# Kernel tuning notes

Hardware: AMD Instinct MI355X
Metric: run time of the kernel (lower is better)

Reference implementation:

```python
import jax, jax.numpy as jnp
import numpy as np
import math

# Model dims (match init_kwargs)
H = 4096      # hidden_size
NH = 32       # num attention heads
NKV = 8       # num kv heads
D = 128       # head_dim
S = 2048      # num tokens
WINDOW = 1024 # sliding window (layer_idx=0 -> active)
SCALE = D ** -0.5
# YaRN rope params from GptOssConfig.rope_parameters
BASE = 500000.0
FACTOR = 4.0
ORIG_MAX = 32768
BETA_FAST = 32
BETA_SLOW = 1


def _yarn_cos_sin(positions):
    """YaRN-scaled rotary cos/sin, NEOX style. Returns ([S, D/2], [S, D/2])."""
    d2 = D // 2
    pos_freqs = BASE ** (np.arange(d2, dtype=np.float64) * 2.0 / D)
    inv_extra = 1.0 / pos_freqs
    inv_inter = 1.0 / (FACTOR * pos_freqs)

    def corr_dim(n):
        return (D * math.log(ORIG_MAX / (n * 2 * math.pi))) / (2 * math.log(BASE))

    low = max(math.floor(corr_dim(BETA_FAST)), 0)
    high = min(math.ceil(corr_dim(BETA_SLOW)), d2 - 1)
    ramp = np.clip((np.arange(d2, dtype=np.float64) - low) / max(high - low, 0.001), 0.0, 1.0)
    mask = 1.0 - ramp  # 1 -> extrapolation (high freq), 0 -> interpolation (low freq)
    inv_freq = inv_inter * (1.0 - mask) + inv_extra * mask
    mscale = 0.1 * math.log(FACTOR) + 1.0
    freqs = positions.astype(jnp.float32)[:, None] * jnp.asarray(inv_freq, dtype=jnp.float32)[None, :]
    return jnp.cos(freqs) * mscale, jnp.sin(freqs) * mscale


def _rope(x, cos, sin):
    # x: [S, h, D]; rotate-halves (NEOX)
    x1, x2 = jnp.split(x, 2, axis=-1)
    c, s = cos[:, None, :], sin[:, None, :]
    return jnp.concatenate([x1 * c - x2 * s, x2 * c + x1 * s], axis=-1)


def reference(hidden_states, positions, qkv_w, qkv_b, o_w, o_b, sinks):
    qs, kvs = NH * D, NKV * D
    qkv = hidden_states @ qkv_w.T + qkv_b                  # [S, qs + 2*kvs]
    q = qkv[:, :qs].reshape(S, NH, D)
    k = qkv[:, qs:qs + kvs].reshape(S, NKV, D)
    v = qkv[:, qs + kvs:].reshape(S, NKV, D)

    cos, sin = _yarn_cos_sin(positions)
    q = _rope(q, cos, sin)
    k = _rope(k, cos, sin)

    # GQA: expand kv heads to match q heads
    g = NH // NKV
    k = jnp.repeat(k, g, axis=1)                            # [S, NH, D]
    v = jnp.repeat(v, g, axis=1)

    scores = jnp.einsum('qhd,khd->hqk', q, k) * SCALE       # [NH, S, S]
    i = jnp.arange(S)[:, None]
    j = jnp.arange(S)[None, :]
    allowed = (j <= i) & ((i - j) < WINDOW)                 # causal + sliding window
    scores = jnp.where(allowed[None, :, :], scores, -jnp.inf)

    # sink-aware softmax: learned per-head sink logit joins the normalization
    m = jnp.maximum(jnp.max(scores, axis=-1), sinks[:, None])   # [NH, S]
    e = jnp.exp(scores - m[..., None])                          # masked -> exp(-inf)=0
    denom = e.sum(-1) + jnp.exp(sinks[:, None] - m)             # [NH, S]
    probs = e / denom[..., None]

    attn = jnp.einsum('hqk,khd->qhd', probs, v).reshape(S, NH * D)
    return attn @ o_w.T + o_b


def setup_inputs() -> dict:
    key = jax.random.key(0)
    k1, k2, k3, k4, k5 = jax.random.split(key, 5)
    w_scale = 0.02
    return {
        'hidden_states': jax.random.normal(k1, (S, H), dtype=jnp.float32),
        'positions': jnp.arange(S, dtype=jnp.int64) if jax.config.jax_enable_x64 else jnp.arange(S, dtype=jnp.int32),
        'qkv_w': jax.random.normal(k2, (NH * D + 2 * NKV * D, H), dtype=jnp.float32) * w_scale,
        'qkv_b': jax.random.normal(k3, (NH * D + 2 * NKV * D,), dtype=jnp.float32) * w_scale,
        'o_w': jax.random.normal(k4, (H, H), dtype=jnp.float32) * w_scale,
        'o_b': jax.random.normal(k5, (H,), dtype=jnp.float32) * w_scale,
        'sinks': jnp.zeros((NH,), dtype=jnp.float32),
    }
```

## Files before the change

### kernel.cpp

```cpp
#include <hip/hip_runtime.h>

#define S_LEN   2048
#define HID     4096
#define NH      32
#define NKV     8
#define HD      128
#define QKV_N   (NH*HD + 2*NKV*HD)
#define WINDOW  1024

typedef unsigned short u16;
typedef short s8v  __attribute__((ext_vector_type(8)));
typedef short s4v  __attribute__((ext_vector_type(4)));
typedef float f4v  __attribute__((ext_vector_type(4)));

#define MFMA16x32(a, b, c) __builtin_amdgcn_mfma_f32_16x16x32_bf16(a, b, c, 0, 0, 0)

typedef __attribute__((address_space(1))) const unsigned int g_u32;
typedef __attribute__((address_space(3))) unsigned int l_u32;

__device__ __forceinline__ float bf2f(u16 h) {
  union { unsigned int u; float f; } x;
  x.u = ((unsigned int)h) << 16;
  return x.f;
}
__device__ __forceinline__ u16 f2bf(float f) {
  union { float f; unsigned int u; } x;
  x.f = f;
  unsigned int u = x.u;
  return (u16)((u + 0x7FFFu + ((u >> 16) & 1u)) >> 16);
}

__global__ __launch_bounds__(256) void cvt_bf16(const float* __restrict__ in,
                                               u16* __restrict__ out) {
  int i = (blockIdx.x * 256 + threadIdx.x) * 4;
  float4 v = *(const float4*)&in[i];
  u16 h[4] = { f2bf(v.x), f2bf(v.y), f2bf(v.z), f2bf(v.w) };
  *(s4v*)&out[i] = *(const s4v*)h;
}

__global__ __launch_bounds__(256) void cvt_fused(
    const float* __restrict__ hidden, const float* __restrict__ qkv_w,
    u16* __restrict__ hb, u16* __restrict__ wW) {
  int b = blockIdx.x;
  const float* in;
  u16* out;
  int i;
  if (b < 24576) { in = qkv_w;  out = wW; i = (b * 256 + threadIdx.x) * 4; }
  else           { in = hidden; out = hb; i = ((b - 24576) * 256 + threadIdx.x) * 4; }
  float4 v = *(const float4*)&in[i];
  u16 h[4] = { f2bf(v.x), f2bf(v.y), f2bf(v.z), f2bf(v.w) };
  *(s4v*)&out[i] = *(const s4v*)h;
}

template<int OUT_BF16>
__global__ __launch_bounds__(512, 4) void gemm_bt(
    const u16* __restrict__ A, const u16* __restrict__ B,
    const float* __restrict__ bias, void* __restrict__ Cp,
    int M, int N, int K)
{
  __shared__ __align__(16) char lds[3 * 24576];
  const int tid  = threadIdx.x;
  const int lane = tid & 63;
  const int w    = tid >> 6;
  const int wm   = w >> 2, wn = w & 3;
  const int ln   = lane & 15, quad = lane >> 4;
  const long mBase = (long)blockIdx.y * 128;
  const long nBase = (long)blockIdx.x * 256;
  const u16* Ab = A + mBase * (long)K;
  const u16* Bb = B + nBase * (long)K;
  const long rs = (long)K * 2;

  f4v acc[4][4];
#pragma unroll
  for (int i = 0; i < 4; ++i)
#pragma unroll
    for (int j = 0; j < 4; ++j)
#pragma unroll
      for (int r = 0; r < 4; ++r) acc[i][j][r] = 0.0f;

  const int nt = K >> 5;

  auto stage = [&](int tile) {
    char* base = lds + (tile % 3) * 24576;
    const int ktb = tile * 64;
#pragma unroll
    for (int k = 0; k < 3; ++k) {
      const u16* gsrc = (k == 0) ? Ab : Bb;
      char* ldst      = (k == 0) ? base : (base + 8192);
      const int kk    = (k == 0) ? 0 : (k - 1);
      int o  = kk * 8192 + w * 1024 + lane * 16;
      int o2 = o ^ ((o >> 3) & 0x30);
      const char* gp = (const char*)gsrc + (long)(o2 >> 6) * rs + ktb + (o2 & 63);
      __builtin_amdgcn_global_load_lds((g_u32*)(const void*)gp,
                                       (l_u32*)(void*)(ldst + kk * 8192 + w * 1024),
                                       16, 0, 0);
    }
  };

  stage(0);
  stage(1);
  asm volatile("s_waitcnt vmcnt(3)" ::: "memory");
  __builtin_amdgcn_s_barrier();
  __builtin_amdgcn_sched_barrier(0);

  int bsel = 0;
  for (int t = 0; t < nt; ++t) {
    char* base = lds + bsel * 24576;
    if (t + 2 < nt) stage(t + 2);

    __builtin_amdgcn_s_setprio(1);
    s8v af[4], bf[4];
#pragma unroll
    for (int f = 0; f < 4; ++f) {
      int r = wm * 64 + f * 16 + ln;
      int o = r * 64 + quad * 16;
      o ^= (o >> 3) & 0x30;
      af[f] = *(const s8v*)(base + o);
    }
#pragma unroll
    for (int j = 0; j < 4; ++j) {
      int r = wn * 64 + j * 16 + ln;
      int o = r * 64 + quad * 16;
      o ^= (o >> 3) & 0x30;
      bf[j] = *(const s8v*)(base + 8192 + o);
    }
#pragma unroll
    for (int i = 0; i < 4; ++i)
#pragma unroll
      for (int j = 0; j < 4; ++j)
        acc[i][j] = MFMA16x32(af[i], bf[j], acc[i][j]);
    __builtin_amdgcn_s_setprio(0);

    if (t < nt - 2) {
      asm volatile("s_waitcnt vmcnt(3)" ::: "memory");
      __builtin_amdgcn_s_barrier();
      __builtin_amdgcn_sched_barrier(0);
    } else if (t == nt - 2) {
      asm volatile("s_waitcnt vmcnt(0)" ::: "memory");
      __builtin_amdgcn_s_barrier();
      __builtin_amdgcn_sched_barrier(0);
    }
    bsel = (bsel == 2) ? 0 : bsel + 1;
  }

#pragma unroll
  for (int i = 0; i < 4; ++i) {
    long rowb = mBase + wm * 64 + i * 16 + quad * 4;
#pragma unroll
    for (int j = 0; j < 4; ++j) {
      long col = nBase + wn * 64 + j * 16 + ln;
      float bv = bias[col];
#pragma unroll
      for (int r = 0; r < 4; ++r) {
        float v = acc[i][j][r] + bv;
        if (OUT_BF16) ((u16*)Cp)[(rowb + r) * (long)N + col] = f2bf(v);
        else          ((float*)Cp)[(rowb + r) * (long)N + col] = v;
      }
    }
  }
}

__global__ __launch_bounds__(256) void rope_split(
    const u16* __restrict__ qkv, const int* __restrict__ positions,
    u16* __restrict__ qo, u16* __restrict__ ko, u16* __restrict__ vo)
{
  const int s = blockIdx.x;
  const int t = threadIdx.x;
  __shared__ float csh[64], snh[64];

  if (t < 64) {
    const double LN_BASE = log(500000.0);
    const double TWO_PI  = 6.283185307179586476925287;
    double cf  = 128.0 * log(32768.0 / (32.0 * TWO_PI)) / (2.0 * LN_BASE);
    double cs_ = 128.0 * log(32768.0 / TWO_PI) / (2.0 * LN_BASE);
    double lowd  = floor(cf);  if (lowd < 0.0)  lowd = 0.0;
    double highd = ceil(cs_);  if (highd > 63.0) highd = 63.0;
    double denom = highd - lowd; if (denom < 0.001) denom = 0.001;
    double d = (double)t;
    double inv_extra = exp(-LN_BASE * d / 64.0);
    double inv_inter = inv_extra * 0.25;
    double ramp = (d - lowd) / denom;
    ramp = ramp < 0.0 ? 0.0 : (ramp > 1.0 ? 1.0 : ramp);
    double maskv = 1.0 - ramp;
    double invf = inv_inter * (1.0 - maskv) + inv_extra * maskv;
    float freq = (float)positions[s] * (float)invf;
    const float msc = 1.1386294361119891f;
    csh[t] = cosf(freq) * msc;
    snh[t] = sinf(freq) * msc;
  }
  __syncthreads();

  const u16* row = qkv + (size_t)s * QKV_N;
  const float SC = 0.08838834764831845f;

#pragma unroll
  for (int i = 0; i < 8; ++i) {
    int p = i * 256 + t;
    int hh = p >> 6, d = p & 63;
    float x1 = bf2f(row[hh * 128 + d]), x2 = bf2f(row[hh * 128 + d + 64]);
    float c = csh[d], sn = snh[d];
    qo[(size_t)s * 4096 + hh * 128 + d]      = f2bf((x1 * c - x2 * sn) * SC);
    qo[(size_t)s * 4096 + hh * 128 + d + 64] = f2bf((x2 * c + x1 * sn) * SC);
  }
#pragma unroll
  for (int i = 0; i < 2; ++i) {
    int p = i * 256 + t;
    int hh = p >> 6, d = p & 63;
    float x1 = bf2f(row[4096 + hh * 128 + d]), x2 = bf2f(row[4096 + hh * 128 + d + 64]);
    float c = csh[d], sn = snh[d];
    ko[(size_t)s * 1024 + hh * 128 + d]      = f2bf(x1 * c - x2 * sn);
    ko[(size_t)s * 1024 + hh * 128 + d + 64] = f2bf(x2 * c + x1 * sn);
  }
#pragma unroll
  for (int i = 0; i < 4; ++i) {
    int e = i * 256 + t;
    vo[(size_t)s * 1024 + e] = row[5120 + e];
  }
}

__global__ __launch_bounds__(256) void transpose_v(const u16* __restrict__ vb,
                                                   u16* __restrict__ vt) {
  __shared__ u16 tile[64][72];
  const int s0 = blockIdx.x * 64, c0 = blockIdx.y * 64;
  const int tid = threadIdx.x;
#pragma unroll
  for (int t = 0; t < 2; ++t) {
    int row = t * 32 + (tid >> 3), col = (tid & 7) * 8;
    *(s8v*)&tile[row][col] = *(const s8v*)&vb[(size_t)(s0 + row) * 1024 + c0 + col];
  }
  __syncthreads();
#pragma unroll
  for (int t = 0; t < 2; ++t) {
    int orow = t * 32 + (tid >> 3), ocol = (tid & 7) * 8;
    u16 v[8];
#pragma unroll
    for (int e = 0; e < 8; ++e) v[e] = tile[ocol + e][orow];
    *(s8v*)&vt[(size_t)(c0 + orow) * 2048 + s0 + ocol] = *(const s8v*)v;
  }
}

__global__ __launch_bounds__(256) void attn_fwd(
    const u16* __restrict__ Q, const u16* __restrict__ Kb,
    const u16* __restrict__ Vt, const float* __restrict__ sinks,
    u16* __restrict__ O)
{
  const int h = blockIdx.y, kvh = h >> 2;
  const int q0 = blockIdx.x * 64;
  const int tid = threadIdx.x, w = tid >> 6, lane = tid & 63;
  const int ln = lane & 15, quad = lane >> 4;
  const int qw = q0 + w * 16;
  const int qi = qw + ln;

  __shared__ __align__(16) u16 sK[64 * 136];
  __shared__ __align__(16) u16 sVt[128 * 72];
  __shared__ __align__(16) u16 sP[4][16 * 72];

  s8v qf[4];
  {
    const u16* qrow = Q + (size_t)qi * 4096 + h * 128;
#pragma unroll
    for (int kb = 0; kb < 4; ++kb)
      qf[kb] = *(const s8v*)&qrow[kb * 32 + quad * 8];
  }

  float m_v = sinks[h], l_v = 1.0f;
  f4v accO[8];
#pragma unroll
  for (int j = 0; j < 8; ++j)
#pragma unroll
    for (int r = 0; r < 4; ++r) accO[j][r] = 0.0f;

  int lo = q0 - (WINDOW - 1); if (lo < 0) lo = 0; lo &= ~63;

  for (int kt = lo; kt <= q0; kt += 64) {
    __syncthreads();
#pragma unroll
    for (int t = 0; t < 4; ++t) {
      int c = t * 256 + tid;
      int row = c >> 4, col = (c & 15) * 8;
      *(s8v*)&sK[row * 136 + col] =
          *(const s8v*)&Kb[(size_t)(kt + row) * 1024 + kvh * 128 + col];
    }
#pragma unroll
    for (int t = 0; t < 4; ++t) {
      int c = t * 256 + tid;
      int row = c >> 3, col = (c & 7) * 8;
      *(s8v*)&sVt[row * 72 + col] =
          *(const s8v*)&Vt[(size_t)(kvh * 128 + row) * 2048 + kt + col];
    }
    __syncthreads();

    f4v sc[4];
    bool dead[4];
#pragma unroll
    for (int h4 = 0; h4 < 4; ++h4) {
      const int kb16 = kt + h4 * 16;
      dead[h4] = (kb16 > qw + 15) || (kb16 + 15 < qw - (WINDOW - 1));
      if (dead[h4]) {
#pragma unroll
        for (int r = 0; r < 4; ++r) sc[h4][r] = -1e30f;
        continue;
      }
      f4v s;
#pragma unroll
      for (int r = 0; r < 4; ++r) s[r] = 0.0f;
#pragma unroll
      for (int kb = 0; kb < 4; ++kb) {
        s8v kf = *(const s8v*)&sK[(h4 * 16 + ln) * 136 + kb * 32 + quad * 8];
        s = MFMA16x32(kf, qf[kb], s);
      }
      const bool full = (kb16 + 15 <= qw) && (qw + 15 - kb16 <= WINDOW - 1);
      if (!full) {
        int base = qi - kb16 - quad * 4;
#pragma unroll
        for (int r = 0; r < 4; ++r)
          s[r] = ((unsigned)(base - r) <= (WINDOW - 1)) ? s[r] : -1e30f;
      }
      sc[h4] = s;
    }

    float mn = m_v;
#pragma unroll
    for (int h4 = 0; h4 < 4; ++h4)
#pragma unroll
      for (int r = 0; r < 4; ++r) mn = fmaxf(mn, sc[h4][r]);
    mn = fmaxf(mn, __shfl_xor(mn, 16));
    mn = fmaxf(mn, __shfl_xor(mn, 32));

    float alpha = __expf(m_v - mn);
    m_v = mn;
    l_v *= alpha;
#pragma unroll
    for (int j = 0; j < 8; ++j)
#pragma unroll
      for (int r = 0; r < 4; ++r) accO[j][r] *= alpha;

    float lsum = 0.0f;
#pragma unroll
    for (int h4 = 0; h4 < 4; ++h4) {
      float p[4];
#pragma unroll
      for (int r = 0; r < 4; ++r) p[r] = __expf(sc[h4][r] - mn);
      lsum += (p[0] + p[1]) + (p[2] + p[3]);
      u16 pb[4] = { f2bf(p[0]), f2bf(p[1]), f2bf(p[2]), f2bf(p[3]) };
      *(s4v*)&sP[w][ln * 72 + h4 * 16 + quad * 4] = *(const s4v*)pb;
    }
    lsum += __shfl_xor(lsum, 16);
    lsum += __shfl_xor(lsum, 32);
    l_v += lsum;

    __syncthreads();

#pragma unroll
    for (int c2 = 0; c2 < 2; ++c2) {
      if (dead[2 * c2] && dead[2 * c2 + 1]) continue;
      s8v pf = *(const s8v*)&sP[w][ln * 72 + c2 * 32 + quad * 8];
#pragma unroll
      for (int j = 0; j < 8; ++j) {
        s8v vf = *(const s8v*)&sVt[(j * 16 + ln) * 72 + c2 * 32 + quad * 8];
        accO[j] = MFMA16x32(vf, pf, accO[j]);
      }
    }
  }

  __syncthreads();
  u16* sO = sK;
  const float rl = 1.0f / l_v;
#pragma unroll
  for (int j = 0; j < 8; ++j) {
    u16 ob[4] = { f2bf(accO[j][0] * rl), f2bf(accO[j][1] * rl),
                  f2bf(accO[j][2] * rl), f2bf(accO[j][3] * rl) };
    *(s4v*)&sO[(w * 16 + ln) * 136 + j * 16 + quad * 4] = *(const s4v*)ob;
  }
  __syncthreads();
  {
    int row = lane >> 2, cc = lane & 3;
#pragma unroll
    for (int i = 0; i < 4; ++i) {
      s8v v = *(const s8v*)&sO[(w * 16 + row) * 136 + cc * 8 + i * 32];
      *(s8v*)&O[(size_t)(q0 + w * 16 + row) * 4096 + h * 128 + cc * 8 + i * 32] = v;
    }
  }
}

extern "C" void kernel_launch(void* const* d_in, const int* in_sizes, int n_in,
                              void* d_out, int out_size, void* d_ws, size_t ws_size,
                              hipStream_t stream) {
  const float* hidden    = (const float*)d_in[0];
  const int*   positions = (const int*)d_in[1];
  const float* qkv_w     = (const float*)d_in[2];
  const float* qkv_b     = (const float*)d_in[3];
  const float* o_w       = (const float*)d_in[4];
  const float* o_b       = (const float*)d_in[5];
  const float* sinks     = (const float*)d_in[6];

  char* ws = (char*)d_ws;
  u16* wW   = (u16*)ws;
  u16* qb   = (u16*)ws;
  u16* kb   = (u16*)(ws + 16777216ull);
  u16* vb   = (u16*)(ws + 20971520ull);
  u16* vt   = (u16*)(ws + 25165824ull);
  u16* attn = (u16*)(ws + 29360128ull);
  u16* hb   = (u16*)(ws + 50331648ull);
  u16* qkvb = (u16*)(ws + 67108864ull);
  u16* oWb  = (u16*)(ws + 50331648ull);

  cvt_fused<<<32768, 256, 0, stream>>>(hidden, qkv_w, hb, wW);

  gemm_bt<1><<<dim3(QKV_N / 256, S_LEN / 128), 512, 0, stream>>>(
      hb, wW, qkv_b, (void*)qkvb, S_LEN, QKV_N, HID);

  rope_split<<<S_LEN, 256, 0, stream>>>(qkvb, positions, qb, kb, vb);

  cvt_bf16<<<16384, 256, 0, stream>>>(o_w, oWb);

  transpose_v<<<dim3(32, 16), 256, 0, stream>>>(vb, vt);

  attn_fwd<<<dim3(S_LEN / 64, NH), 256, 0, stream>>>(qb, kb, vt, sinks, attn);

  gemm_bt<0><<<dim3(HID / 256, S_LEN / 128), 512, 0, stream>>>(
      attn, oWb, o_b, d_out, S_LEN, HID, HID);
}
```

Baseline: 511.7 us.

## Prefetch next K/V tile into registers and drop redundant barriers in attention

The attention loop now loads the next K and V tile into registers while the current tile is computed, then stores them to LDS at the top of the next iteration. Block-wide syncs that only guarded per-warp LDS data are replaced with LDS waitcnts, and MFMA sections get raised wave priority. Separately, the V copy in rope_split is removed and transpose_v reads V directly from the QKV buffer, saving one pass over V. The register prefetch raises VGPR pressure and could reduce occupancy.

```diff
diff --git a/kernel.cpp b/kernel.cpp
--- a/kernel.cpp
+++ b/kernel.cpp
@@ -162,7 +162,7 @@
 
 __global__ __launch_bounds__(256) void rope_split(
     const u16* __restrict__ qkv, const int* __restrict__ positions,
-    u16* __restrict__ qo, u16* __restrict__ ko, u16* __restrict__ vo)
+    u16* __restrict__ qo, u16* __restrict__ ko)
 {
   const int s = blockIdx.x;
   const int t = threadIdx.x;
@@ -211,14 +211,9 @@
     ko[(size_t)s * 1024 + hh * 128 + d]      = f2bf(x1 * c - x2 * sn);
     ko[(size_t)s * 1024 + hh * 128 + d + 64] = f2bf(x2 * c + x1 * sn);
   }
-#pragma unroll
-  for (int i = 0; i < 4; ++i) {
-    int e = i * 256 + t;
-    vo[(size_t)s * 1024 + e] = row[5120 + e];
-  }
-}
-
-__global__ __launch_bounds__(256) void transpose_v(const u16* __restrict__ vb,
+}
+
+__global__ __launch_bounds__(256) void transpose_v(const u16* __restrict__ qkvb,
                                                    u16* __restrict__ vt) {
   __shared__ u16 tile[64][72];
   const int s0 = blockIdx.x * 64, c0 = blockIdx.y * 64;
@@ -226,7 +221,8 @@
 #pragma unroll
   for (int t = 0; t < 2; ++t) {
     int row = t * 32 + (tid >> 3), col = (tid & 7) * 8;
-    *(s8v*)&tile[row][col] = *(const s8v*)&vb[(size_t)(s0 + row) * 1024 + c0 + col];
+    *(s8v*)&tile[row][col] =
+        *(const s8v*)&qkvb[(size_t)(s0 + row) * QKV_N + 5120 + c0 + col];
   }
   __syncthreads();
 #pragma unroll
@@ -272,23 +268,45 @@
 
   int lo = q0 - (WINDOW - 1); if (lo < 0) lo = 0; lo &= ~63;
 
+  s8v kreg[4], vreg[4];
+#pragma unroll
+  for (int t = 0; t < 4; ++t) {
+    int c = t * 256 + tid, row = c >> 4, col = (c & 15) * 8;
+    kreg[t] = *(const s8v*)&Kb[(size_t)(lo + row) * 1024 + kvh * 128 + col];
+  }
+#pragma unroll
+  for (int t = 0; t < 4; ++t) {
+    int c = t * 256 + tid, row = c >> 3, col = (c & 7) * 8;
+    vreg[t] = *(const s8v*)&Vt[(size_t)(kvh * 128 + row) * 2048 + lo + col];
+  }
+
   for (int kt = lo; kt <= q0; kt += 64) {
     __syncthreads();
 #pragma unroll
     for (int t = 0; t < 4; ++t) {
-      int c = t * 256 + tid;
-      int row = c >> 4, col = (c & 15) * 8;
-      *(s8v*)&sK[row * 136 + col] =
-          *(const s8v*)&Kb[(size_t)(kt + row) * 1024 + kvh * 128 + col];
+      int c = t * 256 + tid, row = c >> 4, col = (c & 15) * 8;
+      *(s8v*)&sK[row * 136 + col] = kreg[t];
     }
 #pragma unroll
     for (int t = 0; t < 4; ++t) {
-      int c = t * 256 + tid;
-      int row = c >> 3, col = (c & 7) * 8;
-      *(s8v*)&sVt[row * 72 + col] =
-          *(const s8v*)&Vt[(size_t)(kvh * 128 + row) * 2048 + kt + col];
-    }
-    __syncthreads();
+      int c = t * 256 + tid, row = c >> 3, col = (c & 7) * 8;
+      *(s8v*)&sVt[row * 72 + col] = vreg[t];
+    }
+    if (kt + 64 <= q0) {
+#pragma unroll
+      for (int t = 0; t < 4; ++t) {
+        int c = t * 256 + tid, row = c >> 4, col = (c & 15) * 8;
+        kreg[t] = *(const s8v*)&Kb[(size_t)(kt + 64 + row) * 1024 + kvh * 128 + col];
+      }
+#pragma unroll
+      for (int t = 0; t < 4; ++t) {
+        int c = t * 256 + tid, row = c >> 3, col = (c & 7) * 8;
+        vreg[t] = *(const s8v*)&Vt[(size_t)(kvh * 128 + row) * 2048 + kt + 64 + col];
+      }
+    }
+    asm volatile("s_waitcnt lgkmcnt(0)" ::: "memory");
+    __builtin_amdgcn_sched_barrier(0);
+    __builtin_amdgcn_s_barrier();
 
     f4v sc[4];
     bool dead[4];
@@ -304,11 +322,13 @@
       f4v s;
 #pragma unroll
       for (int r = 0; r < 4; ++r) s[r] = 0.0f;
+      __builtin_amdgcn_s_setprio(1);
 #pragma unroll
       for (int kb = 0; kb < 4; ++kb) {
         s8v kf = *(const s8v*)&sK[(h4 * 16 + ln) * 136 + kb * 32 + quad * 8];
         s = MFMA16x32(kf, qf[kb], s);
       }
+      __builtin_amdgcn_s_setprio(0);
       const bool full = (kb16 + 15 <= qw) && (qw + 15 - kb16 <= WINDOW - 1);
       if (!full) {
         int base = qi - kb16 - quad * 4;
@@ -349,17 +369,20 @@
     lsum += __shfl_xor(lsum, 32);
     l_v += lsum;
 
-    __syncthreads();
+    asm volatile("s_waitcnt lgkmcnt(0)" ::: "memory");
+    __builtin_amdgcn_sched_barrier(0);
 
 #pragma unroll
     for (int c2 = 0; c2 < 2; ++c2) {
       if (dead[2 * c2] && dead[2 * c2 + 1]) continue;
       s8v pf = *(const s8v*)&sP[w][ln * 72 + c2 * 32 + quad * 8];
+      __builtin_amdgcn_s_setprio(1);
 #pragma unroll
       for (int j = 0; j < 8; ++j) {
         s8v vf = *(const s8v*)&sVt[(j * 16 + ln) * 72 + c2 * 32 + quad * 8];
         accO[j] = MFMA16x32(vf, pf, accO[j]);
       }
+      __builtin_amdgcn_s_setprio(0);
     }
   }
 
@@ -372,7 +395,8 @@
                   f2bf(accO[j][2] * rl), f2bf(accO[j][3] * rl) };
     *(s4v*)&sO[(w * 16 + ln) * 136 + j * 16 + quad * 4] = *(const s4v*)ob;
   }
-  __syncthreads();
+  asm volatile("s_waitcnt lgkmcnt(0)" ::: "memory");
+  __builtin_amdgcn_sched_barrier(0);
   {
     int row = lane >> 2, cc = lane & 3;
 #pragma unroll
@@ -398,7 +422,6 @@
   u16* wW   = (u16*)ws;
   u16* qb   = (u16*)ws;
   u16* kb   = (u16*)(ws + 16777216ull);
-  u16* vb   = (u16*)(ws + 20971520ull);
   u16* vt   = (u16*)(ws + 25165824ull);
   u16* attn = (u16*)(ws + 29360128ull);
   u16* hb   = (u16*)(ws + 50331648ull);
@@ -410,11 +433,11 @@
   gemm_bt<1><<<dim3(QKV_N / 256, S_LEN / 128), 512, 0, stream>>>(
       hb, wW, qkv_b, (void*)qkvb, S_LEN, QKV_N, HID);
 
-  rope_split<<<S_LEN, 256, 0, stream>>>(qkvb, positions, qb, kb, vb);
+  rope_split<<<S_LEN, 256, 0, stream>>>(qkvb, positions, qb, kb);
+
+  transpose_v<<<dim3(32, 16), 256, 0, stream>>>(qkvb, vt);
 
   cvt_bf16<<<16384, 256, 0, stream>>>(o_w, oWb);
-
-  transpose_v<<<dim3(32, 16), 256, 0, stream>>>(vb, vt);
 
   attn_fwd<<<dim3(S_LEN / 64, NH), 256, 0, stream>>>(qb, kb, vt, sinks, attn);
 
```

Result: no change. 507.7 us (-0.8%).
